# Kernel optimization log

Measured on AMD Instinct MI355X. Metric: run time of the kernel, lower is better.

Reference implementation:

```python
import jax, jax.numpy as jnp
import numpy as np

DIM, HEADS, FFN, E = 1024, 16, 4096, 8
B, S = 2, 1024
EPS = 1e-5


def _ln(x, g, b):
    mu = jnp.mean(x, axis=-1, keepdims=True)
    var = jnp.mean((x - mu) ** 2, axis=-1, keepdims=True)
    return (x - mu) * jax.lax.rsqrt(var + EPS) * g + b


def setup_inputs() -> dict:
    key = jax.random.key(0)
    ks = jax.random.split(key, 20)
    sd = 0.02
    d, f = DIM, FFN
    return {
        "x": jax.random.normal(ks[0], (B, S, d), jnp.float32),
        "ln1_g": jnp.ones((d,), jnp.float32), "ln1_b": jnp.zeros((d,), jnp.float32),
        "Wqkv": jax.random.normal(ks[1], (d, 3 * d), jnp.float32) * sd,
        "bqkv": jnp.zeros((3 * d,), jnp.float32),
        "Wo": jax.random.normal(ks[2], (d, d), jnp.float32) * sd,
        "bo": jnp.zeros((d,), jnp.float32),
        "ln2_g": jnp.ones((d,), jnp.float32), "ln2_b": jnp.zeros((d,), jnp.float32),
        "gate_w": jax.random.normal(ks[3], (d, E), jnp.float32) * sd,
        "W1": jax.random.normal(ks[4], (E, d, f), jnp.float32) * sd,
        "b1": jnp.zeros((E, f), jnp.float32),
        "W2": jax.random.normal(ks[5], (E, f, d), jnp.float32) * sd,
        "b2": jnp.zeros((E, d), jnp.float32),
        "rW1": jax.random.normal(ks[6], (d, f), jnp.float32) * sd,
        "rb1": jnp.zeros((f,), jnp.float32),
        "rW2": jax.random.normal(ks[7], (f, d), jnp.float32) * sd,
        "rb2": jnp.zeros((d,), jnp.float32),
        "coef_w": jax.random.normal(ks[8], (d, 2), jnp.float32) * sd,
        "coef_b": jnp.zeros((2,), jnp.float32),
    }


def reference(x, ln1_g, ln1_b, Wqkv, bqkv, Wo, bo, ln2_g, ln2_b, gate_w,
              W1, b1, W2, b2, rW1, rb1, rW2, rb2, coef_w, coef_b):
    b, s, d = x.shape
    h, dh = HEADS, d // HEADS

    # --- attention block ---
    xn = _ln(x, ln1_g, ln1_b)
    qkv = xn @ Wqkv + bqkv                       # [b,s,3d]
    q, k, v = jnp.split(qkv, 3, axis=-1)
    q = q.reshape(b, s, h, dh)
    k = k.reshape(b, s, h, dh)
    v = v.reshape(b, s, h, dh)
    scores = jnp.einsum("bqhd,bkhd->bhqk", q, k) / jnp.sqrt(jnp.float32(dh))
    attn = jax.nn.softmax(scores, axis=-1)
    ctx = jnp.einsum("bhqk,bkhd->bqhd", attn, v).reshape(b, s, d)
    x = x + ctx @ Wo + bo

    # --- MoE FFN block (top-1 gating, DeepSpeed residual MoE) ---
    xn2 = _ln(x, ln2_g, ln2_b)
    xt = xn2.reshape(b * s, d)                   # [T,d] tokens
    probs = jax.nn.softmax(xt @ gate_w, axis=-1)  # [T,E]
    gate_val = jnp.max(probs, axis=-1, keepdims=True)   # top-1 prob
    expert_idx = jnp.argmax(probs, axis=-1)
    oh = jax.nn.one_hot(expert_idx, E, dtype=xt.dtype)  # [T,E] dispatch mask

    xe = jnp.einsum("te,td->etd", oh, xt)        # dispatch [E,T,d]
    he = jax.nn.gelu(jnp.einsum("etd,edf->etf", xe, W1) + b1[:, None, :], approximate=False)
    ye = jnp.einsum("etf,efd->etd", he, W2) + b2[:, None, :]
    moe_out = jnp.einsum("te,etd->td", oh, ye) * gate_val  # combine [T,d]

    # residual dense expert + learned mixing coefficient
    rm = jax.nn.gelu(xt @ rW1 + rb1, approximate=False) @ rW2 + rb2
    coef = jax.nn.softmax(xt @ coef_w + coef_b, axis=-1)  # [T,2]
    ff = moe_out * coef[:, 0:1] + rm * coef[:, 1:2]

    return x + ff.reshape(b, s, d)
```

## Files before the change

kernel.cpp:

```cpp
#include <hip/hip_runtime.h>
#include <math.h>

#define TOK 2048
#define NDIM 1024

typedef __attribute__((ext_vector_type(4))) float f32x4;
typedef __attribute__((ext_vector_type(8))) short s16x8;
typedef __attribute__((ext_vector_type(4))) short s16x4;

__device__ __forceinline__ short f2bf(float x) {
  unsigned int u = __builtin_bit_cast(unsigned int, x);
  unsigned int r = (u + 0x7fffu + ((u >> 16) & 1u)) >> 16;
  return (short)r;
}
__device__ __forceinline__ void gload_lds16(const void* g, void* l) {
  __builtin_amdgcn_global_load_lds((const __attribute__((address_space(1))) void*)g,
                                   (__attribute__((address_space(3))) void*)l, 16, 0, 0);
}

struct PackP { const float* src; short* dst; int K, N, nkt; };
__global__ __launch_bounds__(256)
void pack_k(PackP p)
{
  __shared__ short T[64][264];
  const int nkt = p.nkt;
  const int cb = blockIdx.x / nkt, kt = blockIdx.x % nkt;
  const int ntn = p.N >> 6;
  const float* src = p.src + (size_t)blockIdx.y * p.K * p.N + (size_t)(kt * 64) * p.N + cb * 256;
  const int t = threadIdx.x;
  #pragma unroll
  for (int i = 0; i < 16; ++i) {
    const int r = i * 4 + (t >> 6);
    const f32x4 v = *(const f32x4*)(src + (size_t)r * p.N + (t & 63) * 4);
    short* d = &T[r][(t & 63) * 4];
    d[0] = f2bf(v[0]); d[1] = f2bf(v[1]); d[2] = f2bf(v[2]); d[3] = f2bf(v[3]);
  }
  __syncthreads();
  #pragma unroll
  for (int j = 0; j < 4; ++j) {
    short* dst = p.dst + ((size_t)(blockIdx.y * ntn + cb * 4 + j) * nkt + kt) * 4096 + t * 16;
    s16x8 v0, v1;
    #pragma unroll
    for (int jj = 0; jj < 2; ++jj) {
      const int chunk = t * 2 + jj;
      const int col = chunk >> 3, od = chunk & 7, o = od ^ (col & 7);
      #pragma unroll
      for (int kk = 0; kk < 8; ++kk) {
        const short vv = T[o * 8 + kk][j * 64 + col];
        if (jj == 0) v0[kk] = vv; else v1[kk] = vv;
      }
    }
    *(s16x8*)dst = v0;
    *(s16x8*)(dst + 8) = v1;
  }
}

__global__ __launch_bounds__(256)
void ln_k(const float* __restrict__ x, const float* __restrict__ g,
          const float* __restrict__ bb, short* __restrict__ out)
{
  const int row = blockIdx.x, tid = threadIdx.x;
  const f32x4 xv = *(const f32x4*)(x + (size_t)row * NDIM + tid * 4);
  float s = xv[0] + xv[1] + xv[2] + xv[3];
  float s2 = xv[0]*xv[0] + xv[1]*xv[1] + xv[2]*xv[2] + xv[3]*xv[3];
  #pragma unroll
  for (int m = 1; m < 64; m <<= 1) { s += __shfl_xor(s, m); s2 += __shfl_xor(s2, m); }
  __shared__ float red[8];
  const int w = tid >> 6, l = tid & 63;
  if (l == 0) { red[w] = s; red[4 + w] = s2; }
  __syncthreads();
  s = red[0] + red[1] + red[2] + red[3];
  s2 = red[4] + red[5] + red[6] + red[7];
  const float mean = s * (1.0f / NDIM);
  const float var = s2 * (1.0f / NDIM) - mean * mean;
  const float rstd = rsqrtf(var + 1e-5f);
  const f32x4 gv = *(const f32x4*)(g + tid * 4);
  const f32x4 bv = *(const f32x4*)(bb + tid * 4);
  s16x4 ov;
  #pragma unroll
  for (int j = 0; j < 4; ++j) ov[j] = f2bf((xv[j] - mean) * rstd * gv[j] + bv[j]);
  *(s16x4*)(out + (size_t)row * NDIM + tid * 4) = ov;
}

__global__ __launch_bounds__(256)
void gate_k(const float* __restrict__ x1, const float* __restrict__ g,
            const float* __restrict__ bb, const float* __restrict__ gw,
            const float* __restrict__ cw, const float* __restrict__ cb,
            int* __restrict__ counts, int* __restrict__ bucket,
            float* __restrict__ gs, float* __restrict__ c1o)
{
  const int tid = threadIdx.x, l = tid & 63, w = tid >> 6;
  const int t = blockIdx.x * 4 + w;
  f32x4 xv[4];
  #pragma unroll
  for (int it = 0; it < 4; ++it)
    xv[it] = *(const f32x4*)(x1 + (size_t)t * NDIM + it * 256 + l * 4);
  float s = 0.f, s2 = 0.f;
  #pragma unroll
  for (int it = 0; it < 4; ++it)
    #pragma unroll
    for (int j = 0; j < 4; ++j) { s += xv[it][j]; s2 += xv[it][j] * xv[it][j]; }
  #pragma unroll
  for (int m = 1; m < 64; m <<= 1) { s += __shfl_xor(s, m); s2 += __shfl_xor(s2, m); }
  const float mean = s * (1.0f / NDIM);
  const float rstd = rsqrtf(s2 * (1.0f / NDIM) - mean * mean + 1e-5f);
  float acc[10];
  #pragma unroll
  for (int j = 0; j < 10; ++j) acc[j] = 0.f;
  #pragma unroll
  for (int it = 0; it < 4; ++it) {
    #pragma unroll
    for (int j = 0; j < 4; ++j) {
      const int d0 = it * 256 + l * 4 + j;
      const float xn = (xv[it][j] - mean) * rstd * g[d0] + bb[d0];
      const f32x4 g0 = *(const f32x4*)(gw + (size_t)d0 * 8);
      const f32x4 g1 = *(const f32x4*)(gw + (size_t)d0 * 8 + 4);
      #pragma unroll
      for (int q = 0; q < 4; ++q) { acc[q] += xn * g0[q]; acc[4 + q] += xn * g1[q]; }
      acc[8] += xn * cw[d0 * 2]; acc[9] += xn * cw[d0 * 2 + 1];
    }
  }
  #pragma unroll
  for (int j = 0; j < 10; ++j)
    #pragma unroll
    for (int m = 1; m < 64; m <<= 1) acc[j] += __shfl_xor(acc[j], m);
  if (l == 0) {
    int best = 0; float mx = acc[0];
    #pragma unroll
    for (int e = 1; e < 8; ++e) if (acc[e] > mx) { mx = acc[e]; best = e; }
    float se = 0.f;
    #pragma unroll
    for (int e = 0; e < 8; ++e) se += __expf(acc[e] - mx);
    const float gate_val = 1.0f / se;
    const float l0 = acc[8] + cb[0], l1 = acc[9] + cb[1];
    const float cmx = fmaxf(l0, l1);
    const float e0 = __expf(l0 - cmx), e1 = __expf(l1 - cmx);
    const float inv = 1.0f / (e0 + e1);
    const int pos = atomicAdd(&counts[best], 1);
    bucket[best * TOK + pos] = t;
    gs[t] = gate_val * e0 * inv;
    c1o[t] = e1 * inv;
  }
}

struct GemmP {
  const short* A; const short* A2; const short* Bp; const short* Bp2;
  const float* bias; const float* bias2;
  short* outh; short* outh2; float* outf;
  const float* resid; const float* gs; const float* c1;
  const int* bucket; const int* counts;
  int N, K, ktc;
};

template<int MODE>
__global__ __launch_bounds__(256, 3)
void gemm_k(GemmP p)
{
  __shared__ short Al[2][8192];
  __shared__ short Bl[2][4096];
  const int tid = threadIdx.x;
  const int l = tid & 63, w = tid >> 6;
  const int wr = w >> 1, wc = w & 1;
  const int ntn = p.N >> 6, nkt = p.K >> 6;
  const int mt = blockIdx.x / ntn;
  const int nt = blockIdx.x % ntn;
  const int z = blockIdx.z;
  const bool first = (z == 0);
  const int K = p.K, N = p.N;

  int e = 0, cnt = TOK;
  const int* bucket = nullptr;
  if (MODE >= 2) {
    e = blockIdx.y;
    if (e < 8) {
      cnt = p.counts[e];
      if (mt * 128 >= cnt) return;
      bucket = p.bucket + e * TOK;
    }
  }
  const short* Abase = (MODE == 3 && e == 8) ? p.A2 : p.A;
  const float* bias = (MODE >= 2) ? (e < 8 ? p.bias + (size_t)e * N : p.bias2) : p.bias;
  const short* btile = (MODE >= 2)
      ? (e < 8 ? p.Bp + ((size_t)(e * ntn + nt) * nkt) * 4096
               : p.Bp2 + ((size_t)nt * nkt) * 4096)
      : p.Bp + ((size_t)nt * nkt) * 4096;

  const short* aptr[4];
  #pragma unroll
  for (int i = 0; i < 4; ++i) {
    const int rl = (i * 256 + tid) >> 3;
    int row;
    if (bucket) {
      const int bidx = mt * 128 + rl;
      row = bucket[bidx < cnt ? bidx : mt * 128];
    } else row = mt * 128 + rl;
    aptr[i] = Abase + (size_t)row * K + ((tid & 7) ^ (rl & 7)) * 8;
  }

  const int kt0 = z * p.ktc, kt1 = kt0 + p.ktc;

  auto stage = [&](int kt, int buf) {
    const short* bsrc = btile + kt * 4096;
    #pragma unroll
    for (int j = 0; j < 2; ++j)
      gload_lds16(bsrc + (j * 256 + tid) * 8, (char*)Bl[buf] + (j * 256 + (tid & 192)) * 16);
    #pragma unroll
    for (int i = 0; i < 4; ++i)
      gload_lds16(aptr[i] + kt * 64, (char*)Al[buf] + (i * 256 + (tid & 192)) * 16);
  };

  f32x4 acc[4][2] = {};
  stage(kt0, 0);
  for (int kt = kt0; kt < kt1; ++kt) {
    const int cur = (kt - kt0) & 1;
    if (kt + 1 < kt1) {
      stage(kt + 1, cur ^ 1);
      asm volatile("s_waitcnt vmcnt(6)" ::: "memory");
    } else {
      asm volatile("s_waitcnt vmcnt(0)" ::: "memory");
    }
    __builtin_amdgcn_s_barrier();
    #pragma unroll
    for (int ks = 0; ks < 2; ++ks) {
      const int octd = (ks * 4 + (l >> 4)) ^ (l & 7);
      s16x8 af[4], bfr[2];
      #pragma unroll
      for (int mf = 0; mf < 4; ++mf)
        af[mf] = *(const s16x8*)((char*)Al[cur] +
            (wr * 64 + mf * 16 + (l & 15)) * 128 + octd * 16);
      #pragma unroll
      for (int nf = 0; nf < 2; ++nf)
        bfr[nf] = *(const s16x8*)((char*)Bl[cur] +
            (wc * 32 + nf * 16 + (l & 15)) * 128 + octd * 16);
      #pragma unroll
      for (int mf = 0; mf < 4; ++mf)
        #pragma unroll
        for (int nf = 0; nf < 2; ++nf)
          acc[mf][nf] = __builtin_amdgcn_mfma_f32_16x16x32_bf16(af[mf], bfr[nf], acc[mf][nf], 0, 0, 0);
    }
    asm volatile("" ::: "memory");
    __builtin_amdgcn_s_barrier();
  }

  short* oh = (MODE == 2) ? (e < 8 ? p.outh : p.outh2) : p.outh;
  #pragma unroll
  for (int mf = 0; mf < 4; ++mf) {
    #pragma unroll
    for (int i = 0; i < 4; ++i) {
      const int rloc = wr * 64 + mf * 16 + (l >> 4) * 4 + i;
      int grow; bool valid = true;
      if (bucket) {
        const int bidx = mt * 128 + rloc;
        valid = bidx < cnt;
        grow = valid ? bucket[bidx] : 0;
      } else grow = mt * 128 + rloc;
      float srow = 1.f;
      if (MODE == 3) srow = (e < 8) ? (valid ? p.gs[grow] : 0.f) : p.c1[grow];
      #pragma unroll
      for (int nf = 0; nf < 2; ++nf) {
        const int col = nt * 64 + wc * 32 + nf * 16 + (l & 15);
        const size_t off = (size_t)grow * N + col;
        const float bc = first ? bias[col] : 0.f;
        if (MODE == 0) {
          oh[off] = f2bf(acc[mf][nf][i] + bc);
        } else if (MODE == 1) {
          atomicAdd(&p.outf[off], acc[mf][nf][i] + bc + (first ? p.resid[off] : 0.f));
        } else if (MODE == 2) {
          const float v = acc[mf][nf][i] + bc;
          const float gv = 0.5f * v * (1.0f + erff(v * 0.70710678f));
          if (valid) oh[off] = f2bf(gv);
        } else if (MODE == 3) {
          if (valid)
            atomicAdd(&p.outf[off], (acc[mf][nf][i] + bc) * srow +
                      ((e == 8 && first) ? p.resid[off] : 0.f));
        }
      }
    }
  }
}

__global__ __launch_bounds__(256, 2)
void attn_k(const short* __restrict__ qkv, short* __restrict__ ctx)
{
  __shared__ short Klds[64 * 64];
  __shared__ short Vlds[64 * 64];
  __shared__ short Plds[4 * 16 * 64];
  const int tid = threadIdx.x, l = tid & 63, w = tid >> 6;
  const int qt = blockIdx.x;
  const int bh = blockIdx.y;
  const int b = bh >> 4, h = bh & 15;
  const size_t tbase = (size_t)b * 1024;

  const int sq = qt * 64 + w * 16 + (l & 15);
  s16x8 qf[2];
  #pragma unroll
  for (int ks = 0; ks < 2; ++ks)
    qf[ks] = *(const s16x8*)(qkv + (tbase + sq) * 3072 + h * 64 + ks * 32 + (l >> 4) * 8);

  f32x4 o[4] = {};
  float mrow[4], lrow[4];
  #pragma unroll
  for (int i = 0; i < 4; ++i) { mrow[i] = -1e30f; lrow[i] = 0.f; }

  for (int kt = 0; kt < 16; ++kt) {
    #pragma unroll
    for (int i = 0; i < 2; ++i) {
      const int s = i * 256 + tid;
      const int r = s >> 3, c = s & 7, csrc = c ^ (r & 7);
      const short* gsrc = qkv + (tbase + kt * 64 + r) * 3072 + 1024 + h * 64 + csrc * 8;
      gload_lds16(gsrc, (char*)Klds + (i * 256 + (tid & 192)) * 16);
    }
    #pragma unroll
    for (int i = 0; i < 2; ++i) {
      const int kv0 = (i * 4 + w) * 8;
      s16x8 vv;
      #pragma unroll
      for (int j = 0; j < 8; ++j)
        vv[j] = qkv[(tbase + kt * 64 + kv0 + j) * 3072 + 2048 + h * 64 + l];
      *(s16x8*)((char*)Vlds + ((l * 128 + kv0 * 2) ^ ((l & 7) << 4))) = vv;
    }
    __syncthreads();

    f32x4 sv[4];
    #pragma unroll
    for (int nf = 0; nf < 4; ++nf) {
      f32x4 a = {0.f, 0.f, 0.f, 0.f};
      const int kv = nf * 16 + (l & 15);
      #pragma unroll
      for (int ks = 0; ks < 2; ++ks) {
        const s16x8 kb = *(const s16x8*)((char*)Klds +
            ((kv * 128 + (ks * 32 + (l >> 4) * 8) * 2) ^ ((kv & 7) << 4)));
        a = __builtin_amdgcn_mfma_f32_16x16x32_bf16(qf[ks], kb, a, 0, 0, 0);
      }
      sv[nf] = a * 0.125f;
    }
    float sc[4], ps[4];
    #pragma unroll
    for (int i = 0; i < 4; ++i) {
      float m = fmaxf(fmaxf(sv[0][i], sv[1][i]), fmaxf(sv[2][i], sv[3][i]));
      #pragma unroll
      for (int msk = 1; msk < 16; msk <<= 1) m = fmaxf(m, __shfl_xor(m, msk));
      const float mn = fmaxf(mrow[i], m);
      sc[i] = __expf(mrow[i] - mn);
      mrow[i] = mn;
      ps[i] = 0.f;
    }
    #pragma unroll
    for (int nf = 0; nf < 4; ++nf)
      #pragma unroll
      for (int i = 0; i < 4; ++i) {
        const float pp = __expf(sv[nf][i] - mrow[i]);
        sv[nf][i] = pp;
        ps[i] += pp;
      }
    #pragma unroll
    for (int i = 0; i < 4; ++i) {
      #pragma unroll
      for (int msk = 1; msk < 16; msk <<= 1) ps[i] += __shfl_xor(ps[i], msk);
      lrow[i] = lrow[i] * sc[i] + ps[i];
    }
    #pragma unroll
    for (int nf = 0; nf < 4; ++nf)
      #pragma unroll
      for (int i = 0; i < 4; ++i) o[nf][i] *= sc[i];

    char* pw = (char*)Plds + w * 2048;
    #pragma unroll
    for (int nf = 0; nf < 4; ++nf)
      #pragma unroll
      for (int i = 0; i < 4; ++i) {
        const int q = (l >> 4) * 4 + i;
        *(short*)(pw + ((q * 128 + (nf * 16 + (l & 15)) * 2) ^ ((q & 7) << 4))) = f2bf(sv[nf][i]);
      }
    __syncthreads();
    #pragma unroll
    for (int ks = 0; ks < 2; ++ks) {
      const s16x8 pa = *(const s16x8*)(pw +
          (((l & 15) * 128 + (ks * 32 + (l >> 4) * 8) * 2) ^ ((l & 7) << 4)));
      #pragma unroll
      for (int nf = 0; nf < 4; ++nf) {
        const int dh = nf * 16 + (l & 15);
        const s16x8 vb = *(const s16x8*)((char*)Vlds +
            ((dh * 128 + (ks * 32 + (l >> 4) * 8) * 2) ^ ((dh & 7) << 4)));
        o[nf] = __builtin_amdgcn_mfma_f32_16x16x32_bf16(pa, vb, o[nf], 0, 0, 0);
      }
    }
    __syncthreads();
  }
  #pragma unroll
  for (int i = 0; i < 4; ++i) {
    const float inv = 1.0f / lrow[i];
    const size_t t = tbase + qt * 64 + w * 16 + (l >> 4) * 4 + i;
    #pragma unroll
    for (int nf = 0; nf < 4; ++nf)
      ctx[t * 1024 + h * 64 + nf * 16 + (l & 15)] = f2bf(o[nf][i] * inv);
  }
}

extern "C" void kernel_launch(void* const* d_in, const int* in_sizes, int n_in,
                              void* d_out, int out_size, void* d_ws, size_t ws_size,
                              hipStream_t stream)
{
  const float* x    = (const float*)d_in[0];
  const float* ln1g = (const float*)d_in[1];
  const float* ln1b = (const float*)d_in[2];
  const float* Wqkv = (const float*)d_in[3];
  const float* bqkv = (const float*)d_in[4];
  const float* Wo   = (const float*)d_in[5];
  const float* bo   = (const float*)d_in[6];
  const float* ln2g = (const float*)d_in[7];
  const float* ln2b = (const float*)d_in[8];
  const float* gw   = (const float*)d_in[9];
  const float* W1   = (const float*)d_in[10];
  const float* b1   = (const float*)d_in[11];
  const float* W2   = (const float*)d_in[12];
  const float* b2   = (const float*)d_in[13];
  const float* rW1  = (const float*)d_in[14];
  const float* rb1  = (const float*)d_in[15];
  const float* rW2  = (const float*)d_in[16];
  const float* rb2  = (const float*)d_in[17];
  const float* cw   = (const float*)d_in[18];
  const float* cb   = (const float*)d_in[19];
  float* out = (float*)d_out;

  char* ws = (char*)d_ws;
  const size_t MB = 1024 * 1024;
  short* xn1    = (short*)(ws + 0);
  short* qkv    = (short*)(ws + 4 * MB);
  short* he     = (short*)(ws + 4 * MB);
  short* ctx    = (short*)(ws + 16 * MB);
  float* x1     = (float*)(ws + 20 * MB);
  short* xn2    = (short*)(ws + 28 * MB);
  short* hr     = (short*)(ws + 32 * MB);
  int*   counts = (int*)(ws + 56 * MB);
  int*   bucket = (int*)(ws + 56 * MB + 256);
  float* gs     = (float*)(ws + 56 * MB + 256 + 64 * 1024);
  float* c1     = (float*)(ws + 56 * MB + 256 + 64 * 1024 + 8192);
  short* Wqkvp  = (short*)(ws + 64 * MB);
  short* Wop    = (short*)(ws + 70 * MB);
  short* W1p    = (short*)(ws + 72 * MB);
  short* W2p    = (short*)(ws + 136 * MB);
  short* rW1p   = (short*)(ws + 200 * MB);
  short* rW2p   = (short*)(ws + 208 * MB);

  hipMemsetAsync(counts, 0, 8 * sizeof(int), stream);
  hipMemsetAsync(x1, 0, TOK * NDIM * sizeof(float), stream);
  hipMemsetAsync(out, 0, TOK * NDIM * sizeof(float), stream);

  PackP pk;
  pk = PackP{Wqkv, Wqkvp, 1024, 3072, 16}; pack_k<<<dim3(12 * 16, 1), 256, 0, stream>>>(pk);
  pk = PackP{Wo,   Wop,   1024, 1024, 16}; pack_k<<<dim3(4 * 16, 1), 256, 0, stream>>>(pk);
  pk = PackP{W1,   W1p,   1024, 4096, 16}; pack_k<<<dim3(16 * 16, 8), 256, 0, stream>>>(pk);
  pk = PackP{W2,   W2p,   4096, 1024, 64}; pack_k<<<dim3(4 * 64, 8), 256, 0, stream>>>(pk);
  pk = PackP{rW1,  rW1p,  1024, 4096, 16}; pack_k<<<dim3(16 * 16, 1), 256, 0, stream>>>(pk);
  pk = PackP{rW2,  rW2p,  4096, 1024, 64}; pack_k<<<dim3(4 * 64, 1), 256, 0, stream>>>(pk);

  ln_k<<<TOK, 256, 0, stream>>>(x, ln1g, ln1b, xn1);

  GemmP p{};
  p.A = xn1; p.Bp = Wqkvp; p.bias = bqkv; p.outh = qkv; p.N = 3072; p.K = 1024; p.ktc = 16;
  gemm_k<0><<<dim3(16 * 48), 256, 0, stream>>>(p);

  attn_k<<<dim3(16, 32), 256, 0, stream>>>(qkv, ctx);

  p = GemmP{};
  p.A = ctx; p.Bp = Wop; p.bias = bo; p.outf = x1; p.resid = x; p.N = 1024; p.K = 1024; p.ktc = 8;
  gemm_k<1><<<dim3(16 * 16, 1, 2), 256, 0, stream>>>(p);

  ln_k<<<TOK, 256, 0, stream>>>(x1, ln2g, ln2b, xn2);
  gate_k<<<TOK / 4, 256, 0, stream>>>(x1, ln2g, ln2b, gw, cw, cb, counts, bucket, gs, c1);

  p = GemmP{};
  p.A = xn2; p.Bp = W1p; p.Bp2 = rW1p; p.bias = b1; p.bias2 = rb1;
  p.outh = he; p.outh2 = hr; p.N = 4096; p.K = 1024; p.ktc = 16;
  p.bucket = bucket; p.counts = counts;
  gemm_k<2><<<dim3(16 * 64, 9), 256, 0, stream>>>(p);

  p = GemmP{};
  p.A = he; p.A2 = hr; p.Bp = W2p; p.Bp2 = rW2p; p.bias = b2; p.bias2 = rb2;
  p.outf = out; p.resid = x1; p.gs = gs; p.c1 = c1; p.N = 1024; p.K = 4096; p.ktc = 16;
  p.bucket = bucket; p.counts = counts;
  gemm_k<3><<<dim3(16 * 16, 9, 4), 256, 0, stream>>>(p);
}
```

Before: 488.2 us.

## Deepen GEMM prefetch pipeline and drop split-K in MoE down-projection

The GEMM kernel moves from double buffering to a deeper multi-stage pipeline. A is triple-buffered with two tiles in flight, and B is quadruple-buffered with three tiles in flight, using vmcnt waits tuned to the remaining iterations. Occupancy hint drops from 3 to 2 blocks per CU because LDS use grows. The MODE 3 down-projection launch no longer splits K four ways (ktc 64, grid z 1), which removes three quarters of the atomic adds to the output but also cuts block-level parallelism. Because z is now always 0, the residual is added whenever e == 8, without checking first.

```diff
diff --git a/kernel.cpp b/kernel.cpp
--- a/kernel.cpp
+++ b/kernel.cpp
@@ -153,11 +153,11 @@
 };
 
 template<int MODE>
-__global__ __launch_bounds__(256, 3)
+__global__ __launch_bounds__(256, 2)
 void gemm_k(GemmP p)
 {
-  __shared__ short Al[2][8192];
-  __shared__ short Bl[2][4096];
+  __shared__ short Al[3][8192];
+  __shared__ short Bl[4][4096];
   const int tid = threadIdx.x;
   const int l = tid & 63, w = tid >> 6;
   const int wr = w >> 1, wc = w & 1;
@@ -199,26 +199,32 @@
 
   const int kt0 = z * p.ktc, kt1 = kt0 + p.ktc;
 
-  auto stage = [&](int kt, int buf) {
-    const short* bsrc = btile + kt * 4096;
-    #pragma unroll
-    for (int j = 0; j < 2; ++j)
-      gload_lds16(bsrc + (j * 256 + tid) * 8, (char*)Bl[buf] + (j * 256 + (tid & 192)) * 16);
+  auto stageA = [&](int kt, int buf) {
     #pragma unroll
     for (int i = 0; i < 4; ++i)
       gload_lds16(aptr[i] + kt * 64, (char*)Al[buf] + (i * 256 + (tid & 192)) * 16);
   };
+  auto stageB = [&](int kt, int buf) {
+    const short* bsrc = btile + kt * 4096;
+    #pragma unroll
+    for (int j = 0; j < 2; ++j)
+      gload_lds16(bsrc + (j * 256 + tid) * 8, (char*)Bl[buf] + (j * 256 + (tid & 192)) * 16);
+  };
+
+  stageB(kt0, 0); stageA(kt0, 0);
+  stageB(kt0 + 1, 1); stageA(kt0 + 1, 1);
+  stageB(kt0 + 2, 2);
 
   f32x4 acc[4][2] = {};
-  stage(kt0, 0);
+  int curA = 0, curB = 0;
   for (int kt = kt0; kt < kt1; ++kt) {
-    const int cur = (kt - kt0) & 1;
-    if (kt + 1 < kt1) {
-      stage(kt + 1, cur ^ 1);
-      asm volatile("s_waitcnt vmcnt(6)" ::: "memory");
-    } else {
-      asm volatile("s_waitcnt vmcnt(0)" ::: "memory");
-    }
+    const int d = kt1 - kt;
+    if (d > 2) { int wA = curA + 2; if (wA >= 3) wA -= 3; stageA(kt + 2, wA); }
+    if (d > 3) stageB(kt + 3, (curB + 3) & 3);
+    if (d >= 4)      asm volatile("s_waitcnt vmcnt(14)" ::: "memory");
+    else if (d == 3) asm volatile("s_waitcnt vmcnt(12)" ::: "memory");
+    else if (d == 2) asm volatile("s_waitcnt vmcnt(6)" ::: "memory");
+    else             asm volatile("s_waitcnt vmcnt(0)" ::: "memory");
     __builtin_amdgcn_s_barrier();
     #pragma unroll
     for (int ks = 0; ks < 2; ++ks) {
@@ -226,11 +232,11 @@
       s16x8 af[4], bfr[2];
       #pragma unroll
       for (int mf = 0; mf < 4; ++mf)
-        af[mf] = *(const s16x8*)((char*)Al[cur] +
+        af[mf] = *(const s16x8*)((char*)Al[curA] +
             (wr * 64 + mf * 16 + (l & 15)) * 128 + octd * 16);
       #pragma unroll
       for (int nf = 0; nf < 2; ++nf)
-        bfr[nf] = *(const s16x8*)((char*)Bl[cur] +
+        bfr[nf] = *(const s16x8*)((char*)Bl[curB] +
             (wc * 32 + nf * 16 + (l & 15)) * 128 + octd * 16);
       #pragma unroll
       for (int mf = 0; mf < 4; ++mf)
@@ -240,6 +246,8 @@
     }
     asm volatile("" ::: "memory");
     __builtin_amdgcn_s_barrier();
+    curA = (curA == 2) ? 0 : curA + 1;
+    curB = (curB + 1) & 3;
   }
 
   short* oh = (MODE == 2) ? (e < 8 ? p.outh : p.outh2) : p.outh;
@@ -272,7 +280,7 @@
         } else if (MODE == 3) {
           if (valid)
             atomicAdd(&p.outf[off], (acc[mf][nf][i] + bc) * srow +
-                      ((e == 8 && first) ? p.resid[off] : 0.f));
+                      ((e == 8) ? p.resid[off] : 0.f));
         }
       }
     }
@@ -478,7 +486,7 @@
 
   p = GemmP{};
   p.A = he; p.A2 = hr; p.Bp = W2p; p.Bp2 = rW2p; p.bias = b2; p.bias2 = rb2;
-  p.outf = out; p.resid = x1; p.gs = gs; p.c1 = c1; p.N = 1024; p.K = 4096; p.ktc = 16;
+  p.outf = out; p.resid = x1; p.gs = gs; p.c1 = c1; p.N = 1024; p.K = 4096; p.ktc = 64;
   p.bucket = bucket; p.counts = counts;
-  gemm_k<3><<<dim3(16 * 16, 9, 4), 256, 0, stream>>>(p);
-}
+  gemm_k<3><<<dim3(16 * 16, 9, 1), 256, 0, stream>>>(p);
+}
```

After: 548.2 us. 12.3% more time.

## Widen GEMM tiles to 128x128, drop double buffering, add XCD-aware block remap

Applied to the files above, without the earlier changes.

Each GEMM block now computes a 128x128 tile instead of 128x64, so every warp holds a 64x64 accumulator. The weight packing is changed to match, producing 128-column panels. LDS double buffering and the manual vmcnt pipelining are replaced by a single buffer with __syncthreads, and block indices are remapped round-robin in groups of 8, apparently to line up with the chip's XCDs. The W2 GEMM split-K goes from 4 to 2, which cuts atomic traffic but lowers parallelism. Losing load/compute overlap and having fewer blocks (for example 384 for QKV) may hurt latency hiding, while the larger tiles improve data reuse.

```diff
diff --git a/kernel.cpp b/kernel.cpp
--- a/kernel.cpp
+++ b/kernel.cpp
@@ -25,7 +25,7 @@
   __shared__ short T[64][264];
   const int nkt = p.nkt;
   const int cb = blockIdx.x / nkt, kt = blockIdx.x % nkt;
-  const int ntn = p.N >> 6;
+  const int ntn = p.N >> 7;
   const float* src = p.src + (size_t)blockIdx.y * p.K * p.N + (size_t)(kt * 64) * p.N + cb * 256;
   const int t = threadIdx.x;
   #pragma unroll
@@ -37,21 +37,17 @@
   }
   __syncthreads();
   #pragma unroll
-  for (int j = 0; j < 4; ++j) {
-    short* dst = p.dst + ((size_t)(blockIdx.y * ntn + cb * 4 + j) * nkt + kt) * 4096 + t * 16;
-    s16x8 v0, v1;
-    #pragma unroll
-    for (int jj = 0; jj < 2; ++jj) {
-      const int chunk = t * 2 + jj;
-      const int col = chunk >> 3, od = chunk & 7, o = od ^ (col & 7);
-      #pragma unroll
-      for (int kk = 0; kk < 8; ++kk) {
-        const short vv = T[o * 8 + kk][j * 64 + col];
-        if (jj == 0) v0[kk] = vv; else v1[kk] = vv;
-      }
-    }
-    *(s16x8*)dst = v0;
-    *(s16x8*)(dst + 8) = v1;
+  for (int j = 0; j < 2; ++j) {
+    short* dst = p.dst + ((size_t)(blockIdx.y * ntn + cb * 2 + j) * nkt + kt) * 8192;
+    #pragma unroll
+    for (int jj = 0; jj < 4; ++jj) {
+      const int ch = t * 4 + jj;
+      const int col = ch >> 3, od = ch & 7, o = od ^ (col & 7);
+      s16x8 v;
+      #pragma unroll
+      for (int kk = 0; kk < 8; ++kk) v[kk] = T[o * 8 + kk][j * 128 + col];
+      *(s16x8*)(dst + ch * 8) = v;
+    }
   }
 }
 
@@ -149,21 +145,23 @@
   short* outh; short* outh2; float* outf;
   const float* resid; const float* gs; const float* c1;
   const int* bucket; const int* counts;
-  int N, K, ktc;
+  int N, K, ktc, nmt;
 };
 
 template<int MODE>
 __global__ __launch_bounds__(256, 3)
 void gemm_k(GemmP p)
 {
-  __shared__ short Al[2][8192];
-  __shared__ short Bl[2][4096];
+  __shared__ short Al[8192];
+  __shared__ short Bl[8192];
   const int tid = threadIdx.x;
   const int l = tid & 63, w = tid >> 6;
   const int wr = w >> 1, wc = w & 1;
-  const int ntn = p.N >> 6, nkt = p.K >> 6;
-  const int mt = blockIdx.x / ntn;
-  const int nt = blockIdx.x % ntn;
+  const int ntn = p.N >> 7, nkt = p.K >> 6;
+  const int nwg = p.nmt * ntn;
+  const int logical = (blockIdx.x & 7) * (nwg >> 3) + (blockIdx.x >> 3);
+  const int nt = logical / p.nmt;
+  const int mt = logical % p.nmt;
   const int z = blockIdx.z;
   const bool first = (z == 0);
   const int K = p.K, N = p.N;
@@ -181,9 +179,9 @@
   const short* Abase = (MODE == 3 && e == 8) ? p.A2 : p.A;
   const float* bias = (MODE >= 2) ? (e < 8 ? p.bias + (size_t)e * N : p.bias2) : p.bias;
   const short* btile = (MODE >= 2)
-      ? (e < 8 ? p.Bp + ((size_t)(e * ntn + nt) * nkt) * 4096
-               : p.Bp2 + ((size_t)nt * nkt) * 4096)
-      : p.Bp + ((size_t)nt * nkt) * 4096;
+      ? (e < 8 ? p.Bp + ((size_t)(e * ntn + nt) * nkt) * 8192
+               : p.Bp2 + ((size_t)nt * nkt) * 8192)
+      : p.Bp + ((size_t)nt * nkt) * 8192;
 
   const short* aptr[4];
   #pragma unroll
@@ -199,47 +197,35 @@
 
   const int kt0 = z * p.ktc, kt1 = kt0 + p.ktc;
 
-  auto stage = [&](int kt, int buf) {
-    const short* bsrc = btile + kt * 4096;
-    #pragma unroll
-    for (int j = 0; j < 2; ++j)
-      gload_lds16(bsrc + (j * 256 + tid) * 8, (char*)Bl[buf] + (j * 256 + (tid & 192)) * 16);
+  f32x4 acc[4][4] = {};
+  for (int kt = kt0; kt < kt1; ++kt) {
+    const short* bsrc = btile + kt * 8192;
+    #pragma unroll
+    for (int j = 0; j < 4; ++j)
+      gload_lds16(bsrc + (j * 256 + tid) * 8, (char*)Bl + (j * 256 + (tid & 192)) * 16);
     #pragma unroll
     for (int i = 0; i < 4; ++i)
-      gload_lds16(aptr[i] + kt * 64, (char*)Al[buf] + (i * 256 + (tid & 192)) * 16);
-  };
-
-  f32x4 acc[4][2] = {};
-  stage(kt0, 0);
-  for (int kt = kt0; kt < kt1; ++kt) {
-    const int cur = (kt - kt0) & 1;
-    if (kt + 1 < kt1) {
-      stage(kt + 1, cur ^ 1);
-      asm volatile("s_waitcnt vmcnt(6)" ::: "memory");
-    } else {
-      asm volatile("s_waitcnt vmcnt(0)" ::: "memory");
-    }
-    __builtin_amdgcn_s_barrier();
+      gload_lds16(aptr[i] + kt * 64, (char*)Al + (i * 256 + (tid & 192)) * 16);
+    __syncthreads();
     #pragma unroll
     for (int ks = 0; ks < 2; ++ks) {
       const int octd = (ks * 4 + (l >> 4)) ^ (l & 7);
-      s16x8 af[4], bfr[2];
+      s16x8 af[4], bfr[4];
       #pragma unroll
       for (int mf = 0; mf < 4; ++mf)
-        af[mf] = *(const s16x8*)((char*)Al[cur] +
+        af[mf] = *(const s16x8*)((char*)Al +
             (wr * 64 + mf * 16 + (l & 15)) * 128 + octd * 16);
       #pragma unroll
-      for (int nf = 0; nf < 2; ++nf)
-        bfr[nf] = *(const s16x8*)((char*)Bl[cur] +
-            (wc * 32 + nf * 16 + (l & 15)) * 128 + octd * 16);
+      for (int nf = 0; nf < 4; ++nf)
+        bfr[nf] = *(const s16x8*)((char*)Bl +
+            (wc * 64 + nf * 16 + (l & 15)) * 128 + octd * 16);
       #pragma unroll
       for (int mf = 0; mf < 4; ++mf)
         #pragma unroll
-        for (int nf = 0; nf < 2; ++nf)
+        for (int nf = 0; nf < 4; ++nf)
           acc[mf][nf] = __builtin_amdgcn_mfma_f32_16x16x32_bf16(af[mf], bfr[nf], acc[mf][nf], 0, 0, 0);
     }
-    asm volatile("" ::: "memory");
-    __builtin_amdgcn_s_barrier();
+    __syncthreads();
   }
 
   short* oh = (MODE == 2) ? (e < 8 ? p.outh : p.outh2) : p.outh;
@@ -257,8 +243,8 @@
       float srow = 1.f;
       if (MODE == 3) srow = (e < 8) ? (valid ? p.gs[grow] : 0.f) : p.c1[grow];
       #pragma unroll
-      for (int nf = 0; nf < 2; ++nf) {
-        const int col = nt * 64 + wc * 32 + nf * 16 + (l & 15);
+      for (int nf = 0; nf < 4; ++nf) {
+        const int col = nt * 128 + wc * 64 + nf * 16 + (l & 15);
         const size_t off = (size_t)grow * N + col;
         const float bc = first ? bias[col] : 0.f;
         if (MODE == 0) {
@@ -458,27 +444,30 @@
   ln_k<<<TOK, 256, 0, stream>>>(x, ln1g, ln1b, xn1);
 
   GemmP p{};
-  p.A = xn1; p.Bp = Wqkvp; p.bias = bqkv; p.outh = qkv; p.N = 3072; p.K = 1024; p.ktc = 16;
-  gemm_k<0><<<dim3(16 * 48), 256, 0, stream>>>(p);
+  p.A = xn1; p.Bp = Wqkvp; p.bias = bqkv; p.outh = qkv;
+  p.N = 3072; p.K = 1024; p.ktc = 16; p.nmt = 16;
+  gemm_k<0><<<dim3(384), 256, 0, stream>>>(p);
 
   attn_k<<<dim3(16, 32), 256, 0, stream>>>(qkv, ctx);
 
   p = GemmP{};
-  p.A = ctx; p.Bp = Wop; p.bias = bo; p.outf = x1; p.resid = x; p.N = 1024; p.K = 1024; p.ktc = 8;
-  gemm_k<1><<<dim3(16 * 16, 1, 2), 256, 0, stream>>>(p);
+  p.A = ctx; p.Bp = Wop; p.bias = bo; p.outf = x1; p.resid = x;
+  p.N = 1024; p.K = 1024; p.ktc = 8; p.nmt = 16;
+  gemm_k<1><<<dim3(128, 1, 2), 256, 0, stream>>>(p);
 
   ln_k<<<TOK, 256, 0, stream>>>(x1, ln2g, ln2b, xn2);
   gate_k<<<TOK / 4, 256, 0, stream>>>(x1, ln2g, ln2b, gw, cw, cb, counts, bucket, gs, c1);
 
   p = GemmP{};
   p.A = xn2; p.Bp = W1p; p.Bp2 = rW1p; p.bias = b1; p.bias2 = rb1;
-  p.outh = he; p.outh2 = hr; p.N = 4096; p.K = 1024; p.ktc = 16;
+  p.outh = he; p.outh2 = hr; p.N = 4096; p.K = 1024; p.ktc = 16; p.nmt = 16;
   p.bucket = bucket; p.counts = counts;
-  gemm_k<2><<<dim3(16 * 64, 9), 256, 0, stream>>>(p);
+  gemm_k<2><<<dim3(512, 9), 256, 0, stream>>>(p);
 
   p = GemmP{};
   p.A = he; p.A2 = hr; p.Bp = W2p; p.Bp2 = rW2p; p.bias = b2; p.bias2 = rb2;
-  p.outf = out; p.resid = x1; p.gs = gs; p.c1 = c1; p.N = 1024; p.K = 4096; p.ktc = 16;
+  p.outf = out; p.resid = x1; p.gs = gs; p.c1 = c1;
+  p.N = 1024; p.K = 4096; p.ktc = 32; p.nmt = 16;
   p.bucket = bucket; p.counts = counts;
-  gemm_k<3><<<dim3(16 * 16, 9, 4), 256, 0, stream>>>(p);
-}
+  gemm_k<3><<<dim3(128, 9, 2), 256, 0, stream>>>(p);
+}
```

Result: slower. 500.5 us (+2.5%).
